# Optimization experiments

Hardware: AMD Instinct MI355X
Metric: run time of the kernel (lower is better)

Reference implementation:

```python
import math
import jax, jax.numpy as jnp
import numpy as np
from jax import lax

N = 224
EPS_BN = 1e-5


def _conv(x, w, b):
    y = lax.conv_general_dilated(x, w, (1, 1), 'SAME',
                                 dimension_numbers=('NCHW', 'OIHW', 'NCHW'))
    return y + b[None, :, None, None]


def _bn(x, g, beta, m, v):
    # eval-mode BatchNorm2d with running stats
    inv = lax.rsqrt(v + EPS_BN)
    return (x - m[None, :, None, None]) * (g * inv)[None, :, None, None] + beta[None, :, None, None]


def _maxpool2(x):
    return lax.reduce_window(x, -jnp.inf, lax.max, (1, 1, 2, 2), (1, 1, 2, 2), 'VALID')


def setup_inputs() -> dict:
    key = jax.random.key(0)
    ks = jax.random.split(key, 12)
    idx = np.arange(N, dtype=np.float32)
    angles = 2.0 * math.pi * idx[None, :] * idx[:, None] / N
    inp = {
        'sequences': jax.random.normal(ks[0], (16, 8, 3, N, N), dtype=jnp.float32),
        'dft_cos': jnp.asarray(np.cos(angles), dtype=jnp.float32),
        'dft_sin': jnp.asarray(np.sin(angles), dtype=jnp.float32),
        'conv1_w': jax.random.normal(ks[1], (16, 3, 3, 3), dtype=jnp.float32) * 0.1,
        'conv1_b': jnp.zeros((16,), jnp.float32),
        'bn1_g': jnp.ones((16,), jnp.float32),
        'bn1_b': jnp.zeros((16,), jnp.float32),
        'bn1_m': jnp.zeros((16,), jnp.float32),
        'bn1_v': jnp.ones((16,), jnp.float32),
        'conv2_w': jax.random.normal(ks[2], (32, 16, 3, 3), dtype=jnp.float32) * 0.05,
        'conv2_b': jnp.zeros((32,), jnp.float32),
        'bn2_g': jnp.ones((32,), jnp.float32),
        'bn2_b': jnp.zeros((32,), jnp.float32),
        'bn2_m': jnp.zeros((32,), jnp.float32),
        'bn2_v': jnp.ones((32,), jnp.float32),
        'conv3_w': jax.random.normal(ks[3], (64, 32, 3, 3), dtype=jnp.float32) * 0.05,
        'conv3_b': jnp.zeros((64,), jnp.float32),
        'bn3_g': jnp.ones((64,), jnp.float32),
        'bn3_b': jnp.zeros((64,), jnp.float32),
        'bn3_m': jnp.zeros((64,), jnp.float32),
        'bn3_v': jnp.ones((64,), jnp.float32),
        'fc_w': jax.random.normal(ks[4], (128, 64), dtype=jnp.float32) * 0.1,
        'fc_b': jnp.zeros((128,), jnp.float32),
    }
    return inp


def reference(sequences, dft_cos, dft_sin,
              conv1_w, conv1_b, bn1_g, bn1_b, bn1_m, bn1_v,
              conv2_w, conv2_b, bn2_g, bn2_b, bn2_m, bn2_v,
              conv3_w, conv3_b, bn3_g, bn3_b, bn3_m, bn3_v,
              fc_w, fc_b):
    b, s = sequences.shape[0], sequences.shape[1]
    x = sequences[:, s // 2]  # center frames [B,3,H,W]

    # 2D DFT via dense matmul chain: X = (C - jS) x (C - jS)
    C, S = dft_cos, dft_sin
    Cx = jnp.einsum('ij,bcjk->bcik', C, x)
    Sx = jnp.einsum('ij,bcjk->bcik', S, x)
    X_real = jnp.einsum('bcij,jk->bcik', Cx, C) - jnp.einsum('bcij,jk->bcik', Sx, S)
    X_imag = -(jnp.einsum('bcij,jk->bcik', Cx, S) + jnp.einsum('bcij,jk->bcik', Sx, C))
    magnitude = jnp.sqrt(X_real ** 2 + X_imag ** 2 + 1e-08)
    spec = jnp.log(magnitude + 1e-08)
    half = N // 2
    spec = jnp.roll(spec, shift=(half, half), axis=(-2, -1))  # fftshift

    # CNN stack (eval-mode BN, dropout disabled)
    h = jax.nn.relu(_bn(_conv(spec, conv1_w, conv1_b), bn1_g, bn1_b, bn1_m, bn1_v))
    h = _maxpool2(h)
    h = jax.nn.relu(_bn(_conv(h, conv2_w, conv2_b), bn2_g, bn2_b, bn2_m, bn2_v))
    h = _maxpool2(h)
    h = jax.nn.relu(_bn(_conv(h, conv3_w, conv3_b), bn3_g, bn3_b, bn3_m, bn3_v))
    h = jnp.mean(h, axis=(2, 3))  # AdaptiveAvgPool2d((1,1)) + flatten -> [B,64]

    freq_out = jax.nn.relu(h @ fc_w.T + fc_b)  # dropout = identity in eval
    return freq_out
```

## Files before the change

kernel.cpp:

```cpp
#include <hip/hip_runtime.h>
#include <math.h>
#include <stddef.h>

#define N224 224
#define PIX 50176
#define ROWS113 25312

#define OFF_SX    1214976
#define OFF_SPEC  4816896
#define OFF_WT    3211264
#define OFF_WT2   (OFF_WT + 18432)
#define OFF_WT1   (OFF_WT + 23040)
#define OFF_SU3   (OFF_WT + 23472)
#define OFF_SU2   (OFF_WT + 23600)
#define OFF_SU1   (OFF_WT + 23664)
#define OFF_PART  (OFF_WT + 32768)

__global__ __launch_bounds__(256) void prep(
    const float* __restrict__ c1w, const float* __restrict__ c2w,
    const float* __restrict__ c3w, const float* __restrict__ c1b,
    const float* __restrict__ c2b, const float* __restrict__ c3b,
    const float* __restrict__ g1, const float* __restrict__ be1,
    const float* __restrict__ m1, const float* __restrict__ v1,
    const float* __restrict__ g2, const float* __restrict__ be2,
    const float* __restrict__ m2, const float* __restrict__ v2,
    const float* __restrict__ g3, const float* __restrict__ be3,
    const float* __restrict__ m3, const float* __restrict__ v3,
    float* __restrict__ wt3, float* __restrict__ wt2, float* __restrict__ wt1,
    float* __restrict__ su3, float* __restrict__ su2, float* __restrict__ su1)
{
  const int idx = blockIdx.x * 256 + threadIdx.x;
  const int stride = gridDim.x * 256;
  for (int i = idx; i < 18432; i += stride) {
    const int co = i & 63, k = (i >> 6) % 9, cc = i / 576;
    wt3[i] = c3w[co*288 + cc*9 + k];
  }
  for (int i = idx; i < 4608; i += stride) {
    const int co = i & 31, k = (i >> 5) % 9, cc = i / 288;
    wt2[i] = c2w[co*144 + cc*9 + k];
  }
  for (int i = idx; i < 432; i += stride) {
    const int co = i & 15, k = (i >> 4) % 9, cc = i / 144;
    wt1[i] = c1w[co*27 + cc*9 + k];
  }
  if (idx < 64) {
    const float s = g3[idx] * rsqrtf(v3[idx] + 1e-5f);
    su3[idx] = s; su3[64+idx] = (c3b[idx] - m3[idx]) * s + be3[idx];
  } else if (idx < 96) {
    const int c = idx - 64;
    const float s = g2[c] * rsqrtf(v2[c] + 1e-5f);
    su2[c] = s; su2[32+c] = (c2b[c] - m2[c]) * s + be2[c];
  } else if (idx < 112) {
    const int c = idx - 96;
    const float s = g1[c] * rsqrtf(v1[c] + 1e-5f);
    su1[c] = s; su1[16+c] = (c1b[c] - m1[c]) * s + be1[c];
  }
}

__global__ __launch_bounds__(256) void dft1(
    const float* __restrict__ seq, const float* __restrict__ Cm,
    const float* __restrict__ Sm, float* __restrict__ Cx, float* __restrict__ Sx)
{
  const int p = blockIdx.z;
  const int b = p / 3, ch = p % 3;
  const float* __restrict__ x = seq + ((((size_t)b * 8 + 4) * 3 + ch) * PIX);
  const int i0 = blockIdx.y * 32;
  const int k0 = blockIdx.x * 32;
  const int tid = threadIdx.x;
  const int tx = tid & 15, ty = tid >> 4;
  __shared__ float Ctt[16][36], Stt[16][36], Xt[16][36];
  float aC[2][2] = {{0,0},{0,0}}, aS[2][2] = {{0,0},{0,0}};

  const int sidx = tid & 127;
  const int srow = sidx >> 2;
  const int skq  = (sidx & 3) * 4;
  const bool isC = tid < 128;
  const float* __restrict__ csb = (isC ? Cm : Sm) + (size_t)(i0 + srow) * N224 + skq;
  const int xjr = tid >> 4;
  const int xc  = (tid & 15) * 2;
  const float* __restrict__ xb = x + (size_t)xjr * N224 + k0 + xc;

  for (int jt = 0; jt < 14; ++jt) {
    const int j = jt * 16;
    __syncthreads();
    {
      const float4 v = *(const float4*)(csb + j);
      float (*dst)[36] = isC ? Ctt : Stt;
      dst[skq+0][srow] = v.x; dst[skq+1][srow] = v.y;
      dst[skq+2][srow] = v.z; dst[skq+3][srow] = v.w;
      *(float2*)&Xt[xjr][xc] = *(const float2*)(xb + (size_t)j * N224);
    }
    __syncthreads();
#pragma unroll
    for (int jj = 0; jj < 16; ++jj) {
      const float2 cv = *(const float2*)&Ctt[jj][2*ty];
      const float2 sv = *(const float2*)&Stt[jj][2*ty];
      const float2 xv = *(const float2*)&Xt[jj][2*tx];
      aC[0][0] = fmaf(cv.x, xv.x, aC[0][0]); aC[0][1] = fmaf(cv.x, xv.y, aC[0][1]);
      aC[1][0] = fmaf(cv.y, xv.x, aC[1][0]); aC[1][1] = fmaf(cv.y, xv.y, aC[1][1]);
      aS[0][0] = fmaf(sv.x, xv.x, aS[0][0]); aS[0][1] = fmaf(sv.x, xv.y, aS[0][1]);
      aS[1][0] = fmaf(sv.y, xv.x, aS[1][0]); aS[1][1] = fmaf(sv.y, xv.y, aS[1][1]);
    }
  }
  const size_t b113 = (size_t)p * ROWS113;
#pragma unroll
  for (int a = 0; a < 2; ++a) {
    const int i = i0 + 2*ty + a;
    if (i <= 112) {
      const size_t off = b113 + (size_t)i * N224 + k0 + 2*tx;
      *(float2*)&Cx[off] = make_float2(aC[a][0], aC[a][1]);
      *(float2*)&Sx[off] = make_float2(aS[a][0], aS[a][1]);
    }
  }
}

__global__ __launch_bounds__(256) void dft2(
    const float* __restrict__ Cx, const float* __restrict__ Sx,
    const float* __restrict__ Cm, const float* __restrict__ Sm,
    float* __restrict__ spec)
{
  const int p = blockIdx.z;
  const int i0 = blockIdx.y * 32;
  const int k0 = blockIdx.x * 32;
  const int tid = threadIdx.x;
  const int tx = tid & 15, ty = tid >> 4;
  const size_t b113 = (size_t)p * ROWS113;
  __shared__ float CxT[16][36], SxT[16][36], Ct[16][36], St[16][36];
  float p1[2][2] = {{0,0},{0,0}}, p2[2][2] = {{0,0},{0,0}};
  float p3[2][2] = {{0,0},{0,0}}, p4[2][2] = {{0,0},{0,0}};

  const int sidx = tid & 127;
  const int srow = sidx >> 2;
  const int skq  = (sidx & 3) * 4;
  const bool isCx = tid < 128;
  const int ri = (i0 + srow > 112) ? 112 : i0 + srow;
  const float* __restrict__ ab = (isCx ? Cx : Sx) + b113 + (size_t)ri * N224 + skq;
  const int jr = tid >> 4;
  const int cc2 = (tid & 15) * 2;
  const float* __restrict__ cb = Cm + (size_t)jr * N224 + k0 + cc2;
  const float* __restrict__ sb2 = Sm + (size_t)jr * N224 + k0 + cc2;

  for (int jt = 0; jt < 14; ++jt) {
    const int j = jt * 16;
    __syncthreads();
    {
      const float4 v = *(const float4*)(ab + j);
      float (*dst)[36] = isCx ? CxT : SxT;
      dst[skq+0][srow] = v.x; dst[skq+1][srow] = v.y;
      dst[skq+2][srow] = v.z; dst[skq+3][srow] = v.w;
      *(float2*)&Ct[jr][cc2] = *(const float2*)(cb + (size_t)j * N224);
      *(float2*)&St[jr][cc2] = *(const float2*)(sb2 + (size_t)j * N224);
    }
    __syncthreads();
#pragma unroll
    for (int jj = 0; jj < 16; ++jj) {
      const float2 cxv = *(const float2*)&CxT[jj][2*ty];
      const float2 sxv = *(const float2*)&SxT[jj][2*ty];
      const float2 ccv = *(const float2*)&Ct[jj][2*tx];
      const float2 ssv = *(const float2*)&St[jj][2*tx];
      const float cxa[2] = {cxv.x, cxv.y};
      const float sxa[2] = {sxv.x, sxv.y};
      const float cca[2] = {ccv.x, ccv.y};
      const float ssa[2] = {ssv.x, ssv.y};
#pragma unroll
      for (int a = 0; a < 2; ++a)
#pragma unroll
        for (int d = 0; d < 2; ++d) {
          p1[a][d] = fmaf(cxa[a], cca[d], p1[a][d]);
          p2[a][d] = fmaf(sxa[a], ssa[d], p2[a][d]);
          p3[a][d] = fmaf(cxa[a], ssa[d], p3[a][d]);
          p4[a][d] = fmaf(sxa[a], cca[d], p4[a][d]);
        }
    }
  }
  const size_t sb = (size_t)p * PIX;
#pragma unroll
  for (int a = 0; a < 2; ++a) {
    const int i = i0 + 2*ty + a;
    if (i > 112) continue;
    const int shi  = (i < 112) ? i + 112 : i - 112;
    const int shmi = 112 - i;
    const bool irm = (i >= 1) && (i <= 111);
#pragma unroll
    for (int d = 0; d < 2; ++d) {
      const int k = k0 + 2*tx + d;
      if (k > 112) continue;
      const float r1 = p1[a][d] - p2[a][d];
      const float i1 = p3[a][d] + p4[a][d];
      const float sp1v = logf(sqrtf(fmaf(r1, r1, fmaf(i1, i1, 1e-8f))) + 1e-8f);
      const float r2v = p1[a][d] + p2[a][d];
      const float i2v = p3[a][d] - p4[a][d];
      const float sp2v = logf(sqrtf(fmaf(r2v, r2v, fmaf(i2v, i2v, 1e-8f))) + 1e-8f);
      const int shk  = (k < 112) ? k + 112 : k - 112;
      const int shmk = 112 - k;
      const bool krm = (k >= 1) && (k <= 111);
      spec[sb + (size_t)shi*N224 + shk] = sp1v;
      if (irm)        spec[sb + (size_t)shmi*N224 + shk ] = sp2v;
      if (krm)        spec[sb + (size_t)shi *N224 + shmk] = sp2v;
      if (irm && krm) spec[sb + (size_t)shmi*N224 + shmk] = sp1v;
    }
  }
}

__global__ __launch_bounds__(256) void conv1(
    const float* __restrict__ spec, const float* __restrict__ wt1,
    const float* __restrict__ su1, float* __restrict__ out)
{
  const int band = blockIdx.x, b = blockIdx.y;
  const int tid = threadIdx.x;
  const int w = tid >> 6, lane = tid & 63;
  const int co = lane & 15, xsub = lane >> 4;
  __shared__ float in_t[3][6][232];
  for (int i = tid; i < 3*6*232; i += 256) {
    const int c = i % 232, j = (i / 232) % 6, cc = i / 1392;
    const int y = band*4 - 1 + j, gx = c - 1;
    float v = 0.f;
    if (c < 226 && y >= 0 && y < 224 && gx >= 0 && gx < 224)
      v = spec[((size_t)b*3 + cc) * PIX + (size_t)y * N224 + gx];
    in_t[cc][j][c] = v;
  }
  __syncthreads();
  const int pr = w >> 1, xh = w & 1;
  const int X0 = xh*112 + xsub*28;
  const int jb = 2*pr;
  float acc[2][28];
#pragma unroll
  for (int r = 0; r < 2; ++r)
#pragma unroll
    for (int px = 0; px < 28; ++px) acc[r][px] = 0.f;
#pragma unroll
  for (int cc = 0; cc < 3; ++cc) {
    float wr[9];
#pragma unroll
    for (int k = 0; k < 9; ++k) wr[k] = wt1[(cc*9 + k)*16 + co];
#pragma unroll
    for (int rr = 0; rr < 4; ++rr) {
      float xr[32];
      const float4* rp = (const float4*)&in_t[cc][jb+rr][X0];
#pragma unroll
      for (int t = 0; t < 8; ++t) {
        const float4 v = rp[t];
        xr[4*t]=v.x; xr[4*t+1]=v.y; xr[4*t+2]=v.z; xr[4*t+3]=v.w;
      }
#pragma unroll
      for (int cr = 0; cr < 2; ++cr) {
        const int ky = rr - cr;
        if (ky < 0 || ky > 2) continue;
#pragma unroll
        for (int px = 0; px < 28; ++px) {
          acc[cr][px] = fmaf(xr[px  ], wr[ky*3  ], acc[cr][px]);
          acc[cr][px] = fmaf(xr[px+1], wr[ky*3+1], acc[cr][px]);
          acc[cr][px] = fmaf(xr[px+2], wr[ky*3+2], acc[cr][px]);
        }
      }
    }
  }
  const float s = su1[co], u = su1[16+co];
  const int py = band*2 + pr, pxb = X0 >> 1;
#pragma unroll
  for (int p = 0; p < 14; ++p) {
    const float v0 = acc[0][2*p]*s + u,   v1 = acc[0][2*p+1]*s + u;
    const float v2 = acc[1][2*p]*s + u,   v3 = acc[1][2*p+1]*s + u;
    out[(((size_t)b*16 + co)*112 + py)*112 + pxb + p] =
        fmaxf(fmaxf(fmaxf(v0, v1), fmaxf(v2, v3)), 0.f);
  }
}

__global__ __launch_bounds__(256) void conv2(
    const float* __restrict__ h1, const float* __restrict__ wt2,
    const float* __restrict__ su2, float* __restrict__ out)
{
  const int band = blockIdx.x, b = blockIdx.y;
  const int tid = threadIdx.x;
  const int w = tid >> 6, lane = tid & 63;
  const int co = lane & 31, xsub = lane >> 5;
  __shared__ float in_t[16][6][120];
  for (int i = tid; i < 16*6*120; i += 256) {
    const int c = i % 120, j = (i / 120) % 6, cc = i / 720;
    const int y = band*4 - 1 + j, gx = c - 1;
    float v = 0.f;
    if (c < 114 && y >= 0 && y < 112 && gx >= 0 && gx < 112)
      v = h1[(((size_t)b*16 + cc)*112 + y)*112 + gx];
    in_t[cc][j][c] = v;
  }
  __syncthreads();
  const int pr = w >> 1, xh = w & 1;
  const int X0 = xh*56 + xsub*28;
  const int jb = 2*pr;
  float acc[2][28];
#pragma unroll
  for (int r = 0; r < 2; ++r)
#pragma unroll
    for (int px = 0; px < 28; ++px) acc[r][px] = 0.f;
  for (int cc = 0; cc < 16; ++cc) {
    float wr[9];
#pragma unroll
    for (int k = 0; k < 9; ++k) wr[k] = wt2[(cc*9 + k)*32 + co];
#pragma unroll
    for (int rr = 0; rr < 4; ++rr) {
      float xr[32];
      const float4* rp = (const float4*)&in_t[cc][jb+rr][X0];
#pragma unroll
      for (int t = 0; t < 8; ++t) {
        const float4 v = rp[t];
        xr[4*t]=v.x; xr[4*t+1]=v.y; xr[4*t+2]=v.z; xr[4*t+3]=v.w;
      }
#pragma unroll
      for (int cr = 0; cr < 2; ++cr) {
        const int ky = rr - cr;
        if (ky < 0 || ky > 2) continue;
#pragma unroll
        for (int px = 0; px < 28; ++px) {
          acc[cr][px] = fmaf(xr[px  ], wr[ky*3  ], acc[cr][px]);
          acc[cr][px] = fmaf(xr[px+1], wr[ky*3+1], acc[cr][px]);
          acc[cr][px] = fmaf(xr[px+2], wr[ky*3+2], acc[cr][px]);
        }
      }
    }
  }
  const float s = su2[co], u = su2[32+co];
  const int py = band*2 + pr, pxb = X0 >> 1;
#pragma unroll
  for (int p = 0; p < 14; ++p) {
    const float v0 = acc[0][2*p]*s + u,   v1 = acc[0][2*p+1]*s + u;
    const float v2 = acc[1][2*p]*s + u,   v3 = acc[1][2*p+1]*s + u;
    out[(((size_t)b*32 + co)*56 + py)*56 + pxb + p] =
        fmaxf(fmaxf(fmaxf(v0, v1), fmaxf(v2, v3)), 0.f);
  }
}

__global__ __launch_bounds__(256) void conv3(
    const float* __restrict__ h2, const float* __restrict__ wt3,
    const float* __restrict__ su3, float* __restrict__ part)
{
  const int band = blockIdx.x, b = blockIdx.y;
  const int tid = threadIdx.x;
  const int w = tid >> 6, co = tid & 63;
  __shared__ float in_t[32][4][60];
  for (int i = tid; i < 32*4*60; i += 256) {
    const int c = i % 60, j = (i / 60) % 4, cc = i / 240;
    const int y = band*2 - 1 + j, gx = c - 1;
    float v = 0.f;
    if (c < 58 && y >= 0 && y < 56 && gx >= 0 && gx < 56)
      v = h2[(((size_t)b*32 + cc)*56 + y)*56 + gx];
    in_t[cc][j][c] = v;
  }
  __syncthreads();
  const int rb = w >> 1, xh = w & 1;
  const int X0 = xh * 28;
  float acc[28];
#pragma unroll
  for (int px = 0; px < 28; ++px) acc[px] = 0.f;
  for (int cc = 0; cc < 32; ++cc) {
    float wr[9];
#pragma unroll
    for (int k = 0; k < 9; ++k) wr[k] = wt3[(cc*9 + k)*64 + co];
#pragma unroll
    for (int rr = 0; rr < 3; ++rr) {
      float xr[32];
      const float4* rp = (const float4*)&in_t[cc][rb+rr][X0];
#pragma unroll
      for (int t = 0; t < 8; ++t) {
        const float4 v = rp[t];
        xr[4*t]=v.x; xr[4*t+1]=v.y; xr[4*t+2]=v.z; xr[4*t+3]=v.w;
      }
#pragma unroll
      for (int px = 0; px < 28; ++px) {
        acc[px] = fmaf(xr[px  ], wr[rr*3  ], acc[px]);
        acc[px] = fmaf(xr[px+1], wr[rr*3+1], acc[px]);
        acc[px] = fmaf(xr[px+2], wr[rr*3+2], acc[px]);
      }
    }
  }
  const float s = su3[co], u = su3[64+co];
  float sum = 0.f;
#pragma unroll
  for (int px = 0; px < 28; ++px)
    sum += fmaxf(acc[px]*s + u, 0.f);
  part[((size_t)b*64 + co)*112 + band*4 + w] = sum;
}

__global__ __launch_bounds__(128) void mean_fc(
    const float* __restrict__ part, const float* __restrict__ fw,
    const float* __restrict__ fb, float* __restrict__ out)
{
  const int b = blockIdx.x;
  const int tid = threadIdx.x;
  __shared__ float h3s[64];
  if (tid < 64) {
    float s = 0.f;
    const float* pp = part + ((size_t)b*64 + tid)*112;
#pragma unroll
    for (int i = 0; i < 112; ++i) s += pp[i];
    h3s[tid] = s * (1.0f / 3136.0f);
  }
  __syncthreads();
  float acc = fb[tid];
#pragma unroll
  for (int c = 0; c < 64; ++c)
    acc = fmaf(h3s[c], fw[tid*64 + c], acc);
  out[b*128 + tid] = fmaxf(acc, 0.f);
}

extern "C" void kernel_launch(void* const* d_in, const int* in_sizes, int n_in,
                              void* d_out, int out_size, void* d_ws, size_t ws_size,
                              hipStream_t stream) {
  const float* seq  = (const float*)d_in[0];
  const float* dcos = (const float*)d_in[1];
  const float* dsin = (const float*)d_in[2];
  const float* c1w  = (const float*)d_in[3];
  const float* c1b  = (const float*)d_in[4];
  const float* b1g  = (const float*)d_in[5];
  const float* b1b  = (const float*)d_in[6];
  const float* b1m  = (const float*)d_in[7];
  const float* b1v  = (const float*)d_in[8];
  const float* c2w  = (const float*)d_in[9];
  const float* c2b  = (const float*)d_in[10];
  const float* b2g  = (const float*)d_in[11];
  const float* b2b  = (const float*)d_in[12];
  const float* b2m  = (const float*)d_in[13];
  const float* b2v  = (const float*)d_in[14];
  const float* c3w  = (const float*)d_in[15];
  const float* c3b  = (const float*)d_in[16];
  const float* b3g  = (const float*)d_in[17];
  const float* b3b  = (const float*)d_in[18];
  const float* b3m  = (const float*)d_in[19];
  const float* b3v  = (const float*)d_in[20];
  const float* fw   = (const float*)d_in[21];
  const float* fb   = (const float*)d_in[22];
  float* out = (float*)d_out;

  float* ws   = (float*)d_ws;
  float* Cx   = ws;
  float* Sx   = ws + OFF_SX;
  float* spec = ws + OFF_SPEC;
  float* h1   = ws;
  float* h2   = ws + OFF_SPEC;
  float* wt3  = ws + OFF_WT;
  float* wt2  = ws + OFF_WT2;
  float* wt1  = ws + OFF_WT1;
  float* su3  = ws + OFF_SU3;
  float* su2  = ws + OFF_SU2;
  float* su1  = ws + OFF_SU1;
  float* part = ws + OFF_PART;

  prep<<<24, 256, 0, stream>>>(c1w, c2w, c3w, c1b, c2b, c3b,
                               b1g, b1b, b1m, b1v, b2g, b2b, b2m, b2v,
                               b3g, b3b, b3m, b3v, wt3, wt2, wt1, su3, su2, su1);
  dft1<<<dim3(7, 4, 48), 256, 0, stream>>>(seq, dcos, dsin, Cx, Sx);
  dft2<<<dim3(4, 4, 48), 256, 0, stream>>>(Cx, Sx, dcos, dsin, spec);
  conv1<<<dim3(56, 16), 256, 0, stream>>>(spec, wt1, su1, h1);
  conv2<<<dim3(28, 16), 256, 0, stream>>>(h1, wt2, su2, h2);
  conv3<<<dim3(28, 16), 256, 0, stream>>>(h2, wt3, su3, part);
  mean_fc<<<16, 128, 0, stream>>>(part, fw, fb, out);
}
```

Measured before the change: 191.3 us.

## Shrink per-thread conv tiles to double block counts and use shuffle pooling

Each conv kernel now computes fewer output rows or pixels per thread, and the grid grows to match: conv1 goes to 112 bands, conv2 to a 2x56x16 grid, conv3 to 56 bands. The two pooled rows are now computed by different lanes and combined with a cross-lane shuffle max. The aim is to raise occupancy and use more CUs on the small 16-image batch by cutting register-heavy accumulators. In exchange, overlapping halo rows are reloaded more often, conv3 needs an extra shared-memory reduction, and the redundant row loads per output rise.

```diff
diff --git a/kernel.cpp b/kernel.cpp
--- a/kernel.cpp
+++ b/kernel.cpp
@@ -208,61 +208,60 @@
 {
   const int band = blockIdx.x, b = blockIdx.y;
   const int tid = threadIdx.x;
-  const int w = tid >> 6, lane = tid & 63;
-  const int co = lane & 15, xsub = lane >> 4;
-  __shared__ float in_t[3][6][232];
-  for (int i = tid; i < 3*6*232; i += 256) {
-    const int c = i % 232, j = (i / 232) % 6, cc = i / 1392;
-    const int y = band*4 - 1 + j, gx = c - 1;
+  const int lane = tid & 63, w = tid >> 6;
+  const int co = lane & 15, cr = (lane >> 4) & 1, xs = lane >> 5;
+  const int xh = w >> 1, xq = w & 1;
+  __shared__ float in_t[3][4][232];
+  for (int i = tid; i < 3*4*232; i += 256) {
+    const int c = i % 232, r = (i / 232) % 4, cc = i / 928;
+    const int y = band*2 - 1 + r, gx = c - 1;
     float v = 0.f;
     if (c < 226 && y >= 0 && y < 224 && gx >= 0 && gx < 224)
       v = spec[((size_t)b*3 + cc) * PIX + (size_t)y * N224 + gx];
-    in_t[cc][j][c] = v;
+    in_t[cc][r][c] = v;
   }
   __syncthreads();
-  const int pr = w >> 1, xh = w & 1;
-  const int X0 = xh*112 + xsub*28;
-  const int jb = 2*pr;
-  float acc[2][28];
-#pragma unroll
-  for (int r = 0; r < 2; ++r)
-#pragma unroll
-    for (int px = 0; px < 28; ++px) acc[r][px] = 0.f;
+  const int X0 = xh*112 + xq*56 + xs*28;
+  float acc[28];
+#pragma unroll
+  for (int px = 0; px < 28; ++px) acc[px] = 0.f;
 #pragma unroll
   for (int cc = 0; cc < 3; ++cc) {
     float wr[9];
 #pragma unroll
     for (int k = 0; k < 9; ++k) wr[k] = wt1[(cc*9 + k)*16 + co];
 #pragma unroll
-    for (int rr = 0; rr < 4; ++rr) {
+    for (int ky = 0; ky < 3; ++ky) {
       float xr[32];
-      const float4* rp = (const float4*)&in_t[cc][jb+rr][X0];
+      const float4* rp = (const float4*)&in_t[cc][cr + ky][X0];
 #pragma unroll
       for (int t = 0; t < 8; ++t) {
         const float4 v = rp[t];
         xr[4*t]=v.x; xr[4*t+1]=v.y; xr[4*t+2]=v.z; xr[4*t+3]=v.w;
       }
 #pragma unroll
-      for (int cr = 0; cr < 2; ++cr) {
-        const int ky = rr - cr;
-        if (ky < 0 || ky > 2) continue;
-#pragma unroll
-        for (int px = 0; px < 28; ++px) {
-          acc[cr][px] = fmaf(xr[px  ], wr[ky*3  ], acc[cr][px]);
-          acc[cr][px] = fmaf(xr[px+1], wr[ky*3+1], acc[cr][px]);
-          acc[cr][px] = fmaf(xr[px+2], wr[ky*3+2], acc[cr][px]);
-        }
+      for (int px = 0; px < 28; ++px) {
+        acc[px] = fmaf(xr[px  ], wr[ky*3  ], acc[px]);
+        acc[px] = fmaf(xr[px+1], wr[ky*3+1], acc[px]);
+        acc[px] = fmaf(xr[px+2], wr[ky*3+2], acc[px]);
       }
     }
   }
   const float s = su1[co], u = su1[16+co];
-  const int py = band*2 + pr, pxb = X0 >> 1;
+  float m[14];
+#pragma unroll
+  for (int p = 0; p < 14; ++p)
+    m[p] = fmaxf(acc[2*p]*s + u, acc[2*p+1]*s + u);
 #pragma unroll
   for (int p = 0; p < 14; ++p) {
-    const float v0 = acc[0][2*p]*s + u,   v1 = acc[0][2*p+1]*s + u;
-    const float v2 = acc[1][2*p]*s + u,   v3 = acc[1][2*p+1]*s + u;
-    out[(((size_t)b*16 + co)*112 + py)*112 + pxb + p] =
-        fmaxf(fmaxf(fmaxf(v0, v1), fmaxf(v2, v3)), 0.f);
+    const float pm = __shfl_xor(m[p], 16);
+    m[p] = fmaxf(fmaxf(m[p], pm), 0.f);
+  }
+  if (cr == 0) {
+    const int pxb = X0 >> 1;
+    float* op = &out[(((size_t)b*16 + co)*112 + band)*112 + pxb];
+#pragma unroll
+    for (int p = 0; p < 14; ++p) op[p] = m[p];
   }
 }
 
@@ -270,62 +269,59 @@
     const float* __restrict__ h1, const float* __restrict__ wt2,
     const float* __restrict__ su2, float* __restrict__ out)
 {
-  const int band = blockIdx.x, b = blockIdx.y;
-  const int tid = threadIdx.x;
-  const int w = tid >> 6, lane = tid & 63;
-  const int co = lane & 31, xsub = lane >> 5;
-  __shared__ float in_t[16][6][120];
-  for (int i = tid; i < 16*6*120; i += 256) {
-    const int c = i % 120, j = (i / 120) % 6, cc = i / 720;
-    const int y = band*4 - 1 + j, gx = c - 1;
+  const int xh = blockIdx.x, band = blockIdx.y, b = blockIdx.z;
+  const int tid = threadIdx.x;
+  const int lane = tid & 63, w = tid >> 6;
+  const int co = lane & 31, cr = lane >> 5;
+  __shared__ float in_t[16][4][64];
+  for (int i = tid; i < 16*4*58; i += 256) {
+    const int c = i % 58, r = (i / 58) % 4, cc = i / 232;
+    const int y = band*2 - 1 + r, gx = xh*56 - 1 + c;
     float v = 0.f;
-    if (c < 114 && y >= 0 && y < 112 && gx >= 0 && gx < 112)
+    if (y >= 0 && y < 112 && gx >= 0 && gx < 112)
       v = h1[(((size_t)b*16 + cc)*112 + y)*112 + gx];
-    in_t[cc][j][c] = v;
+    in_t[cc][r][c] = v;
   }
   __syncthreads();
-  const int pr = w >> 1, xh = w & 1;
-  const int X0 = xh*56 + xsub*28;
-  const int jb = 2*pr;
-  float acc[2][28];
-#pragma unroll
-  for (int r = 0; r < 2; ++r)
-#pragma unroll
-    for (int px = 0; px < 28; ++px) acc[r][px] = 0.f;
+  const int X0 = w * 14;
+  float acc[14];
+#pragma unroll
+  for (int px = 0; px < 14; ++px) acc[px] = 0.f;
   for (int cc = 0; cc < 16; ++cc) {
     float wr[9];
 #pragma unroll
     for (int k = 0; k < 9; ++k) wr[k] = wt2[(cc*9 + k)*32 + co];
 #pragma unroll
-    for (int rr = 0; rr < 4; ++rr) {
-      float xr[32];
-      const float4* rp = (const float4*)&in_t[cc][jb+rr][X0];
+    for (int ky = 0; ky < 3; ++ky) {
+      float xr[16];
+      const float2* rp = (const float2*)&in_t[cc][cr + ky][X0];
 #pragma unroll
       for (int t = 0; t < 8; ++t) {
-        const float4 v = rp[t];
-        xr[4*t]=v.x; xr[4*t+1]=v.y; xr[4*t+2]=v.z; xr[4*t+3]=v.w;
-      }
-#pragma unroll
-      for (int cr = 0; cr < 2; ++cr) {
-        const int ky = rr - cr;
-        if (ky < 0 || ky > 2) continue;
-#pragma unroll
-        for (int px = 0; px < 28; ++px) {
-          acc[cr][px] = fmaf(xr[px  ], wr[ky*3  ], acc[cr][px]);
-          acc[cr][px] = fmaf(xr[px+1], wr[ky*3+1], acc[cr][px]);
-          acc[cr][px] = fmaf(xr[px+2], wr[ky*3+2], acc[cr][px]);
-        }
+        const float2 v = rp[t];
+        xr[2*t] = v.x; xr[2*t+1] = v.y;
+      }
+#pragma unroll
+      for (int px = 0; px < 14; ++px) {
+        acc[px] = fmaf(xr[px  ], wr[ky*3  ], acc[px]);
+        acc[px] = fmaf(xr[px+1], wr[ky*3+1], acc[px]);
+        acc[px] = fmaf(xr[px+2], wr[ky*3+2], acc[px]);
       }
     }
   }
   const float s = su2[co], u = su2[32+co];
-  const int py = band*2 + pr, pxb = X0 >> 1;
-#pragma unroll
-  for (int p = 0; p < 14; ++p) {
-    const float v0 = acc[0][2*p]*s + u,   v1 = acc[0][2*p+1]*s + u;
-    const float v2 = acc[1][2*p]*s + u,   v3 = acc[1][2*p+1]*s + u;
-    out[(((size_t)b*32 + co)*56 + py)*56 + pxb + p] =
-        fmaxf(fmaxf(fmaxf(v0, v1), fmaxf(v2, v3)), 0.f);
+  float m[7];
+#pragma unroll
+  for (int p = 0; p < 7; ++p)
+    m[p] = fmaxf(acc[2*p]*s + u, acc[2*p+1]*s + u);
+#pragma unroll
+  for (int p = 0; p < 7; ++p) {
+    const float pm = __shfl_xor(m[p], 32);
+    m[p] = fmaxf(fmaxf(m[p], pm), 0.f);
+  }
+  if (cr == 0) {
+    float* op = &out[(((size_t)b*32 + co)*56 + band)*56 + xh*28 + w*7];
+#pragma unroll
+    for (int p = 0; p < 7; ++p) op[p] = m[p];
   }
 }
 
@@ -335,37 +331,37 @@
 {
   const int band = blockIdx.x, b = blockIdx.y;
   const int tid = threadIdx.x;
-  const int w = tid >> 6, co = tid & 63;
-  __shared__ float in_t[32][4][60];
-  for (int i = tid; i < 32*4*60; i += 256) {
-    const int c = i % 60, j = (i / 60) % 4, cc = i / 240;
-    const int y = band*2 - 1 + j, gx = c - 1;
+  const int co = tid & 63, w = tid >> 6;
+  __shared__ float in_t[32][3][64];
+  __shared__ float red[4][64];
+  for (int i = tid; i < 32*3*58; i += 256) {
+    const int c = i % 58, r = (i / 58) % 3, cc = i / 174;
+    const int y = band - 1 + r, gx = c - 1;
     float v = 0.f;
-    if (c < 58 && y >= 0 && y < 56 && gx >= 0 && gx < 56)
+    if (y >= 0 && y < 56 && gx >= 0 && gx < 56)
       v = h2[(((size_t)b*32 + cc)*56 + y)*56 + gx];
-    in_t[cc][j][c] = v;
+    in_t[cc][r][c] = v;
   }
   __syncthreads();
-  const int rb = w >> 1, xh = w & 1;
-  const int X0 = xh * 28;
-  float acc[28];
-#pragma unroll
-  for (int px = 0; px < 28; ++px) acc[px] = 0.f;
+  const int X0 = w * 14;
+  float acc[14];
+#pragma unroll
+  for (int px = 0; px < 14; ++px) acc[px] = 0.f;
   for (int cc = 0; cc < 32; ++cc) {
     float wr[9];
 #pragma unroll
     for (int k = 0; k < 9; ++k) wr[k] = wt3[(cc*9 + k)*64 + co];
 #pragma unroll
     for (int rr = 0; rr < 3; ++rr) {
-      float xr[32];
-      const float4* rp = (const float4*)&in_t[cc][rb+rr][X0];
+      float xr[16];
+      const float2* rp = (const float2*)&in_t[cc][rr][X0];
 #pragma unroll
       for (int t = 0; t < 8; ++t) {
-        const float4 v = rp[t];
-        xr[4*t]=v.x; xr[4*t+1]=v.y; xr[4*t+2]=v.z; xr[4*t+3]=v.w;
-      }
-#pragma unroll
-      for (int px = 0; px < 28; ++px) {
+        const float2 v = rp[t];
+        xr[2*t] = v.x; xr[2*t+1] = v.y;
+      }
+#pragma unroll
+      for (int px = 0; px < 14; ++px) {
         acc[px] = fmaf(xr[px  ], wr[rr*3  ], acc[px]);
         acc[px] = fmaf(xr[px+1], wr[rr*3+1], acc[px]);
         acc[px] = fmaf(xr[px+2], wr[rr*3+2], acc[px]);
@@ -375,9 +371,13 @@
   const float s = su3[co], u = su3[64+co];
   float sum = 0.f;
 #pragma unroll
-  for (int px = 0; px < 28; ++px)
+  for (int px = 0; px < 14; ++px)
     sum += fmaxf(acc[px]*s + u, 0.f);
-  part[((size_t)b*64 + co)*112 + band*4 + w] = sum;
+  red[w][co] = sum;
+  __syncthreads();
+  if (tid < 64)
+    part[((size_t)b*64 + co)*56 + band] =
+        red[0][co] + red[1][co] + red[2][co] + red[3][co];
 }
 
 __global__ __launch_bounds__(128) void mean_fc(
@@ -389,9 +389,9 @@
   __shared__ float h3s[64];
   if (tid < 64) {
     float s = 0.f;
-    const float* pp = part + ((size_t)b*64 + tid)*112;
-#pragma unroll
-    for (int i = 0; i < 112; ++i) s += pp[i];
+    const float* pp = part + ((size_t)b*64 + tid)*56;
+#pragma unroll
+    for (int i = 0; i < 56; ++i) s += pp[i];
     h3s[tid] = s * (1.0f / 3136.0f);
   }
   __syncthreads();
@@ -449,8 +449,8 @@
                                b3g, b3b, b3m, b3v, wt3, wt2, wt1, su3, su2, su1);
   dft1<<<dim3(7, 4, 48), 256, 0, stream>>>(seq, dcos, dsin, Cx, Sx);
   dft2<<<dim3(4, 4, 48), 256, 0, stream>>>(Cx, Sx, dcos, dsin, spec);
-  conv1<<<dim3(56, 16), 256, 0, stream>>>(spec, wt1, su1, h1);
-  conv2<<<dim3(28, 16), 256, 0, stream>>>(h1, wt2, su2, h2);
-  conv3<<<dim3(28, 16), 256, 0, stream>>>(h2, wt3, su3, part);
+  conv1<<<dim3(112, 16), 256, 0, stream>>>(spec, wt1, su1, h1);
+  conv2<<<dim3(2, 56, 16), 256, 0, stream>>>(h1, wt2, su2, h2);
+  conv3<<<dim3(56, 16), 256, 0, stream>>>(h2, wt3, su3, part);
   mean_fc<<<16, 128, 0, stream>>>(part, fw, fb, out);
 }
```

New measurement: 164.0 us. 1.17x faster.
